# Optimization experiments

Measured on AMD Instinct MI355X. Metric: run time of the kernel, lower is better.

## Reference

```python
import jax, jax.numpy as jnp
import numpy as np

NUM_AGENTS = 8
OBSERVATION_SIZE = 30
INPUT_SHAPE = 4 + 2 * OBSERVATION_SIZE  # 64
STATE_SHAPE = INPUT_SHAPE * NUM_AGENTS  # 512
HYPER_HIDDEN_DIM = 40
QMIX_HIDDEN_DIM = 40


def setup_inputs() -> dict:
    key = jax.random.key(0)
    ks = jax.random.split(key, 16)
    E, T = 256, 256

    def lin(k, fan_in, fan_out):
        kw, kb = jax.random.split(k)
        bound = 1.0 / np.sqrt(fan_in)
        w = jax.random.uniform(kw, (fan_in, fan_out), jnp.float32, -bound, bound)
        b = jax.random.uniform(kb, (fan_out,), jnp.float32, -bound, bound)
        return w, b

    hw1_w0, hw1_b0 = lin(ks[0], STATE_SHAPE, HYPER_HIDDEN_DIM)
    hw1_w1, hw1_b1 = lin(ks[1], HYPER_HIDDEN_DIM, NUM_AGENTS * QMIX_HIDDEN_DIM)
    hw2_w0, hw2_b0 = lin(ks[2], STATE_SHAPE, HYPER_HIDDEN_DIM)
    hw2_w1, hw2_b1 = lin(ks[3], HYPER_HIDDEN_DIM, QMIX_HIDDEN_DIM)
    hb1_w, hb1_b = lin(ks[4], STATE_SHAPE, QMIX_HIDDEN_DIM)
    hb2_w0, hb2_b0 = lin(ks[5], STATE_SHAPE, QMIX_HIDDEN_DIM)
    hb2_w1, hb2_b1 = lin(ks[6], QMIX_HIDDEN_DIM, 1)

    return {
        "q_values": jax.random.normal(ks[7], (E, T, NUM_AGENTS), jnp.float32),
        "states": jax.random.normal(ks[8], (E, T, STATE_SHAPE), jnp.float32),
        "hw1_w0": hw1_w0, "hw1_b0": hw1_b0, "hw1_w1": hw1_w1, "hw1_b1": hw1_b1,
        "hw2_w0": hw2_w0, "hw2_b0": hw2_b0, "hw2_w1": hw2_w1, "hw2_b1": hw2_b1,
        "hb1_w": hb1_w, "hb1_b": hb1_b,
        "hb2_w0": hb2_w0, "hb2_b0": hb2_b0, "hb2_w1": hb2_w1, "hb2_b1": hb2_b1,
    }


def reference(q_values, states, hw1_w0, hw1_b0, hw1_w1, hw1_b1,
              hw2_w0, hw2_b0, hw2_w1, hw2_b1,
              hb1_w, hb1_b, hb2_w0, hb2_b0, hb2_w1, hb2_b1):
    E = q_values.shape[0]
    q = q_values.reshape(-1, NUM_AGENTS)          # [B, A]
    s = states.reshape(-1, STATE_SHAPE)           # [B, S]

    # hyper_w1: Linear-ReLU-Linear -> abs -> [B, A, H]
    w1 = jnp.abs(jax.nn.relu(s @ hw1_w0 + hw1_b0) @ hw1_w1 + hw1_b1)
    w1 = w1.reshape(-1, NUM_AGENTS, QMIX_HIDDEN_DIM)
    b1 = s @ hb1_w + hb1_b                        # [B, H]

    hidden = jax.nn.elu(jnp.einsum('ba,bah->bh', q, w1) + b1)  # [B, H]

    # hyper_w2 -> abs -> [B, H]; hyper_b2 -> [B, 1]
    w2 = jnp.abs(jax.nn.relu(s @ hw2_w0 + hw2_b0) @ hw2_w1 + hw2_b1)
    b2 = jax.nn.relu(s @ hb2_w0 + hb2_b0) @ hb2_w1 + hb2_b1    # [B, 1]

    q_total = jnp.einsum('bh,bh->b', hidden, w2)[:, None] + b2  # [B, 1]
    return q_total.reshape(E, -1, 1)
```

## Files before the change

kernel.cpp:

```cpp
#include <hip/hip_runtime.h>
#include <math.h>

#define NA 8
#define SS 512
#define BROWS 32
#define NTHREADS 320

typedef __attribute__((ext_vector_type(8))) short bf16x8;
typedef __attribute__((ext_vector_type(4))) float f32x4;

static __device__ __forceinline__ unsigned short f2bf(float f) {
    union { float f; unsigned u; } v; v.f = f;
    unsigned r = v.u + 0x7FFFu + ((v.u >> 16) & 1u);
    return (unsigned short)(r >> 16);
}
static __device__ __forceinline__ float bf2f(unsigned short u) {
    union { unsigned u; float f; } v; v.u = ((unsigned)u) << 16; return v.f;
}

#define BP_OFF   0
#define BP1_OFF  81920
#define BP2_OFF  102400
#define BIAS0_BYTE 210944

__global__ void prep_kernel(const float* __restrict__ hw1_w0, const float* __restrict__ hb1_w,
                            const float* __restrict__ hw2_w0, const float* __restrict__ hb2_w0,
                            const float* __restrict__ hw1_w1, const float* __restrict__ hw2_w1,
                            const float* __restrict__ hw1_b0, const float* __restrict__ hb1_b,
                            const float* __restrict__ hw2_b0, const float* __restrict__ hb2_b0,
                            unsigned short* __restrict__ ws16, float* __restrict__ bias0) {
    int idx = blockIdx.x * blockDim.x + threadIdx.x;
    if (idx < 81920) {
        int i = idx & 7, l = (idx >> 3) & 63, t = idx >> 9;
        int kt = t & 15, nt = t >> 4;
        int k = kt * 32 + (l >> 4) * 8 + i;
        int n = nt * 16 + (l & 15);
        int seg = n / 40, c = n - seg * 40;
        const float* src = (seg == 0) ? hw1_w0 : (seg == 1) ? hb1_w : (seg == 2) ? hw2_w0 : hb2_w0;
        ws16[BP_OFF + idx] = f2bf(src[k * 40 + c]);
    } else if (idx < 81920 + 20480) {
        int j = idx - 81920;
        int i = j & 7, l = (j >> 3) & 63, t = j >> 9;
        int kt = t & 1, nt = t >> 1;
        int k = kt * 32 + (l >> 4) * 8 + i;
        int n = nt * 16 + (l & 15);
        float v = (k < 40) ? hw1_w1[k * 320 + n] : 0.f;
        ws16[BP1_OFF + j] = f2bf(v);
    } else if (idx < 81920 + 20480 + 3072) {
        int j = idx - 102400;
        int i = j & 7, l = (j >> 3) & 63, t = j >> 9;
        int kt = t & 1, nt = t >> 1;
        int k = kt * 32 + (l >> 4) * 8 + i;
        int n = nt * 16 + (l & 15);
        float v = (k < 40 && n < 40) ? hw2_w1[k * 40 + n] : 0.f;
        ws16[BP2_OFF + j] = f2bf(v);
    } else if (idx < 81920 + 20480 + 3072 + 160) {
        int j = idx - 105472;
        int seg = j / 40, c = j - seg * 40;
        const float* b = (seg == 0) ? hw1_b0 : (seg == 1) ? hb1_b : (seg == 2) ? hw2_b0 : hb2_b0;
        bias0[j] = b[c];
    }
}

#define W1_STRIDE 324
#define B1_OFF    32768
#define H1_OFF    38400
#define H2_OFF    42496
#define W2_OFF    46592
#define B2_OFF    49152
#define SMEM_BYTES 49408

__global__ __launch_bounds__(NTHREADS, 4) void qmix_kernel(
    const float* __restrict__ q_values, const float* __restrict__ states,
    const unsigned short* __restrict__ Bp, const unsigned short* __restrict__ Bp1,
    const unsigned short* __restrict__ Bp2, const float* __restrict__ bias0,
    const float* __restrict__ hw1_b1, const float* __restrict__ hw2_b1,
    const float* __restrict__ hb2_w1, const float* __restrict__ hb2_b1,
    float* __restrict__ out)
{
    __shared__ __align__(16) char smem[SMEM_BYTES];
    const int tid = threadIdx.x;
    const int wv = tid >> 6;
    const int l = tid & 63;
    const int p = l & 15;
    const int row0 = blockIdx.x * BROWS;

    {
        const float4* sg = (const float4*)(states + (size_t)row0 * SS);
        for (int idx = tid; idx < BROWS * (SS / 4); idx += NTHREADS) {
            int r = idx >> 7;
            int c4 = idx & 127;
            float4 v = sg[idx];
            ushort4 b;
            b.x = f2bf(v.x); b.y = f2bf(v.y); b.z = f2bf(v.z); b.w = f2bf(v.w);
            int byte = (r * 1024 + c4 * 8) ^ ((r & 7) << 4);
            *(ushort4*)(smem + byte) = b;
        }
        for (int idx = tid; idx < 32 * 24; idx += NTHREADS) {
            int r = idx / 24, k = 40 + (idx - r * 24);
            int byte = (r * 128 + k * 2) ^ ((r & 7) << 4);
            *(unsigned short*)(smem + H1_OFF + byte) = 0;
            *(unsigned short*)(smem + H2_OFF + byte) = 0;
        }
    }
    __syncthreads();

    f32x4 acc[2][2] = {};
    {
        const int kch = (l >> 4) * 16;
        const int r0 = p;
        const int r1 = r0 + 16;
        const int swz0 = (r0 & 7) << 4;
        const unsigned short* bp0 = Bp + (size_t)((wv * 2 + 0) * 16) * 512 + (size_t)l * 8;
        const unsigned short* bp1 = Bp + (size_t)((wv * 2 + 1) * 16) * 512 + (size_t)l * 8;
        #pragma unroll
        for (int kt = 0; kt < 16; ++kt) {
            bf16x8 a0 = *(const bf16x8*)(smem + ((r0 * 1024 + kt * 64 + kch) ^ swz0));
            bf16x8 a1 = *(const bf16x8*)(smem + ((r1 * 1024 + kt * 64 + kch) ^ swz0));
            bf16x8 b0 = *(const bf16x8*)(bp0 + kt * 512);
            bf16x8 b1 = *(const bf16x8*)(bp1 + kt * 512);
            acc[0][0] = __builtin_amdgcn_mfma_f32_16x16x32_bf16(a0, b0, acc[0][0], 0, 0, 0);
            acc[0][1] = __builtin_amdgcn_mfma_f32_16x16x32_bf16(a0, b1, acc[0][1], 0, 0, 0);
            acc[1][0] = __builtin_amdgcn_mfma_f32_16x16x32_bf16(a1, b0, acc[1][0], 0, 0, 0);
            acc[1][1] = __builtin_amdgcn_mfma_f32_16x16x32_bf16(a1, b1, acc[1][1], 0, 0, 0);
        }
    }

    {
        float rs[2][4] = {{0.f,0.f,0.f,0.f},{0.f,0.f,0.f,0.f}};
        float* b1buf = (float*)(smem + B1_OFF);
        #pragma unroll
        for (int ntl = 0; ntl < 2; ++ntl) {
            const int c = wv * 32 + ntl * 16 + p;
            const float bia = bias0[c];
            const float hbw = (c >= 120) ? hb2_w1[c - 120] : 0.f;
            #pragma unroll
            for (int mt = 0; mt < 2; ++mt)
            #pragma unroll
            for (int g = 0; g < 4; ++g) {
                const int row = mt * 16 + (l >> 4) * 4 + g;
                const float v = acc[mt][ntl][g] + bia;
                if (c < 40) {
                    *(unsigned short*)(smem + H1_OFF + ((row * 128 + c * 2) ^ ((row & 7) << 4)))
                        = f2bf(fmaxf(v, 0.f));
                } else if (c < 80) {
                    b1buf[row * 44 + (c - 40)] = v;
                } else if (c < 120) {
                    *(unsigned short*)(smem + H2_OFF + ((row * 128 + (c - 80) * 2) ^ ((row & 7) << 4)))
                        = f2bf(fmaxf(v, 0.f));
                } else {
                    rs[mt][g] += fmaxf(v, 0.f) * hbw;
                }
            }
        }
        if (wv >= 3) {
            float* B2 = (float*)(smem + B2_OFF);
            #pragma unroll
            for (int mt = 0; mt < 2; ++mt)
            #pragma unroll
            for (int g = 0; g < 4; ++g) {
                float r2 = rs[mt][g];
                r2 += __shfl_xor(r2, 1);
                r2 += __shfl_xor(r2, 2);
                r2 += __shfl_xor(r2, 4);
                r2 += __shfl_xor(r2, 8);
                if (p == 0) B2[(wv - 3) * 32 + mt * 16 + (l >> 4) * 4 + g] = r2;
            }
        }
    }
    __syncthreads();

    {
        char* H1 = smem + H1_OFF;
        const int kch = (l >> 4) * 16;
        f32x4 wacc[2][4] = {};
        #pragma unroll
        for (int kt = 0; kt < 2; ++kt) {
            bf16x8 a[2];
            #pragma unroll
            for (int mt = 0; mt < 2; ++mt) {
                int row = mt * 16 + p;
                a[mt] = *(const bf16x8*)(H1 + ((row * 128 + kt * 64 + kch) ^ ((row & 7) << 4)));
            }
            #pragma unroll
            for (int t = 0; t < 4; ++t) {
                int nt1 = wv * 4 + t;
                bf16x8 b = *(const bf16x8*)(Bp1 + ((size_t)(nt1 * 2 + kt) * 64 + l) * 8);
                wacc[0][t] = __builtin_amdgcn_mfma_f32_16x16x32_bf16(a[0], b, wacc[0][t], 0, 0, 0);
                wacc[1][t] = __builtin_amdgcn_mfma_f32_16x16x32_bf16(a[1], b, wacc[1][t], 0, 0, 0);
            }
        }
        unsigned short* W1 = (unsigned short*)smem;
        #pragma unroll
        for (int mt = 0; mt < 2; ++mt)
        #pragma unroll
        for (int t = 0; t < 4; ++t)
        #pragma unroll
        for (int g = 0; g < 4; ++g) {
            int row = mt * 16 + (l >> 4) * 4 + g;
            int n = (wv * 4 + t) * 16 + p;
            W1[row * W1_STRIDE + n] = f2bf(fabsf(wacc[mt][t][g] + hw1_b1[n]));
        }
        if (wv < 3) {
            char* H2 = smem + H2_OFF;
            f32x4 c2[2] = {};
            #pragma unroll
            for (int kt = 0; kt < 2; ++kt) {
                bf16x8 a[2];
                #pragma unroll
                for (int mt = 0; mt < 2; ++mt) {
                    int row = mt * 16 + p;
                    a[mt] = *(const bf16x8*)(H2 + ((row * 128 + kt * 64 + kch) ^ ((row & 7) << 4)));
                }
                bf16x8 b = *(const bf16x8*)(Bp2 + ((size_t)(wv * 2 + kt) * 64 + l) * 8);
                c2[0] = __builtin_amdgcn_mfma_f32_16x16x32_bf16(a[0], b, c2[0], 0, 0, 0);
                c2[1] = __builtin_amdgcn_mfma_f32_16x16x32_bf16(a[1], b, c2[1], 0, 0, 0);
            }
            unsigned short* W2 = (unsigned short*)(smem + W2_OFF);
            #pragma unroll
            for (int mt = 0; mt < 2; ++mt)
            #pragma unroll
            for (int g = 0; g < 4; ++g) {
                int row = mt * 16 + (l >> 4) * 4 + g;
                int n = wv * 16 + p;
                if (n < 40) W2[row * 40 + n] = f2bf(fabsf(c2[mt][g] + hw2_b1[n]));
            }
        }
    }
    __syncthreads();

    {
        float* b1buf = (float*)(smem + B1_OFF);
        unsigned short* W1 = (unsigned short*)smem;
        unsigned short* W2 = (unsigned short*)(smem + W2_OFF);
        float* PR = (float*)(smem + H1_OFF);
        int r = tid / 10;
        int hb_ = tid - r * 10;
        const float4* qp = (const float4*)(q_values + (size_t)(row0 + r) * NA);
        float4 qa = qp[0], qb = qp[1];
        float qv[8] = {qa.x, qa.y, qa.z, qa.w, qb.x, qb.y, qb.z, qb.w};
        float psum = 0.f;
        #pragma unroll
        for (int kk = 0; kk < 4; ++kk) {
            int h = hb_ + kk * 10;
            float acc2 = b1buf[r * 44 + h];
            #pragma unroll
            for (int a = 0; a < 8; ++a) acc2 += qv[a] * bf2f(W1[r * W1_STRIDE + a * 40 + h]);
            float hid = (acc2 > 0.f) ? acc2 : expm1f(acc2);
            psum += hid * bf2f(W2[r * 40 + h]);
        }
        PR[tid] = psum;
    }
    __syncthreads();
    if (tid < 32) {
        float* PR = (float*)(smem + H1_OFF);
        float* B2 = (float*)(smem + B2_OFF);
        float s = B2[tid] + B2[32 + tid] + hb2_b1[0];
        #pragma unroll
        for (int g = 0; g < 10; ++g) s += PR[tid * 10 + g];
        out[row0 + tid] = s;
    }
}

extern "C" void kernel_launch(void* const* d_in, const int* in_sizes, int n_in,
                              void* d_out, int out_size, void* d_ws, size_t ws_size,
                              hipStream_t stream) {
    const float* q_values = (const float*)d_in[0];
    const float* states   = (const float*)d_in[1];
    const float* hw1_w0 = (const float*)d_in[2];
    const float* hw1_b0 = (const float*)d_in[3];
    const float* hw1_w1 = (const float*)d_in[4];
    const float* hw1_b1 = (const float*)d_in[5];
    const float* hw2_w0 = (const float*)d_in[6];
    const float* hw2_b0 = (const float*)d_in[7];
    const float* hw2_w1 = (const float*)d_in[8];
    const float* hw2_b1 = (const float*)d_in[9];
    const float* hb1_w  = (const float*)d_in[10];
    const float* hb1_b  = (const float*)d_in[11];
    const float* hb2_w0 = (const float*)d_in[12];
    const float* hb2_b0 = (const float*)d_in[13];
    const float* hb2_w1 = (const float*)d_in[14];
    const float* hb2_b1 = (const float*)d_in[15];

    unsigned short* ws16 = (unsigned short*)d_ws;
    float* bias0 = (float*)((char*)d_ws + BIAS0_BYTE);

    const int prep_total = 81920 + 20480 + 3072 + 160;
    prep_kernel<<<(prep_total + 255) / 256, 256, 0, stream>>>(
        hw1_w0, hb1_w, hw2_w0, hb2_w0, hw1_w1, hw2_w1,
        hw1_b0, hb1_b, hw2_b0, hb2_b0, ws16, bias0);

    const int B = in_sizes[0] / NA;
    qmix_kernel<<<B / BROWS, NTHREADS, 0, stream>>>(
        q_values, states,
        ws16 + BP_OFF, ws16 + BP1_OFF, ws16 + BP2_OFF, bias0,
        hw1_b1, hw2_b1, hb2_w1, hb2_b1, (float*)d_out);
}
```

Baseline: 268.7 us.

## Rewrite qmix kernel as single-wave 16-row blocks with register-resident A operand

Replaces the 320-thread, 32-row block with a single 64-lane wave handling 16 rows. States are loaded straight from global into bf16 MFMA A-fragments held in registers rather than staged through LDS. Biases are folded into the accumulator initialisation, the W1 result is consumed in registers through a bucketed q-weighted reduction, and all __syncthreads are removed. Each wave now streams the full hyper-weight matrix on its own, so weight reads per row double and register pressure rises in exchange for less LDS traffic and no block barriers.

```diff
diff --git a/kernel.cpp b/kernel.cpp
--- a/kernel.cpp
+++ b/kernel.cpp
@@ -3,8 +3,6 @@
 
 #define NA 8
 #define SS 512
-#define BROWS 32
-#define NTHREADS 320
 
 typedef __attribute__((ext_vector_type(8))) short bf16x8;
 typedef __attribute__((ext_vector_type(4))) float f32x4;
@@ -16,6 +14,10 @@
 }
 static __device__ __forceinline__ float bf2f(unsigned short u) {
     union { unsigned u; float f; } v; v.u = ((unsigned)u) << 16; return v.f;
+}
+static __device__ __forceinline__ unsigned pkhu(float x, float y) {
+    union { float f; unsigned u; } a, b; a.f = x; b.f = y;
+    return ((a.u + 0x8000u) >> 16) | ((b.u + 0x8000u) & 0xFFFF0000u);
 }
 
 #define BP_OFF   0
@@ -62,15 +64,14 @@
     }
 }
 
-#define W1_STRIDE 324
-#define B1_OFF    32768
-#define H1_OFF    38400
-#define H2_OFF    42496
-#define W2_OFF    46592
-#define B2_OFF    49152
-#define SMEM_BYTES 49408
-
-__global__ __launch_bounds__(NTHREADS, 4) void qmix_kernel(
+#define LDS_H1 0
+#define LDS_H2 2048
+#define LDS_B1 4096
+#define LDS_W2 6720
+#define LDS_QB 8000
+#define SMEM_BYTES 8512
+
+__global__ __launch_bounds__(64, 4) void qmix_kernel(
     const float* __restrict__ q_values, const float* __restrict__ states,
     const unsigned short* __restrict__ Bp, const unsigned short* __restrict__ Bp1,
     const unsigned short* __restrict__ Bp2, const float* __restrict__ bias0,
@@ -79,186 +80,206 @@
     float* __restrict__ out)
 {
     __shared__ __align__(16) char smem[SMEM_BYTES];
-    const int tid = threadIdx.x;
-    const int wv = tid >> 6;
-    const int l = tid & 63;
-    const int p = l & 15;
-    const int row0 = blockIdx.x * BROWS;
-
+    const int l = threadIdx.x;
+    const int s = l & 15;
+    const int g4 = l >> 4;
+    const int row0 = blockIdx.x * 16;
+
+    if (l < 32) {
+        float4 v = *(const float4*)(q_values + (size_t)row0 * NA + l * 4);
+        *(float4*)(smem + LDS_QB + l * 16) = v;
+    }
+    #pragma unroll
+    for (int i = 0; i < 6; ++i) {
+        int idx = i * 64 + l;
+        int r = idx / 24, k = 40 + idx % 24;
+        int byte = (r * 128 + k * 2) ^ ((r & 7) << 4);
+        *(unsigned short*)(smem + LDS_H1 + byte) = 0;
+        *(unsigned short*)(smem + LDS_H2 + byte) = 0;
+    }
+
+    const float* Ap = states + (size_t)(row0 + s) * SS + g4 * 8;
+    bf16x8 aB[16];
     {
-        const float4* sg = (const float4*)(states + (size_t)row0 * SS);
-        for (int idx = tid; idx < BROWS * (SS / 4); idx += NTHREADS) {
-            int r = idx >> 7;
-            int c4 = idx & 127;
-            float4 v = sg[idx];
-            ushort4 b;
-            b.x = f2bf(v.x); b.y = f2bf(v.y); b.z = f2bf(v.z); b.w = f2bf(v.w);
-            int byte = (r * 1024 + c4 * 8) ^ ((r & 7) << 4);
-            *(ushort4*)(smem + byte) = b;
-        }
-        for (int idx = tid; idx < 32 * 24; idx += NTHREADS) {
-            int r = idx / 24, k = 40 + (idx - r * 24);
-            int byte = (r * 128 + k * 2) ^ ((r & 7) << 4);
-            *(unsigned short*)(smem + H1_OFF + byte) = 0;
-            *(unsigned short*)(smem + H2_OFF + byte) = 0;
-        }
-    }
-    __syncthreads();
-
-    f32x4 acc[2][2] = {};
+        float4 wx[4], wy[4];
+        #pragma unroll
+        for (int d = 0; d < 4; ++d) {
+            wx[d] = *(const float4*)(Ap + d * 32);
+            wy[d] = *(const float4*)(Ap + d * 32 + 4);
+        }
+        #pragma unroll
+        for (int kt = 0; kt < 16; ++kt) {
+            float4 x = wx[kt & 3], y = wy[kt & 3];
+            if (kt + 4 < 16) {
+                wx[kt & 3] = *(const float4*)(Ap + (kt + 4) * 32);
+                wy[kt & 3] = *(const float4*)(Ap + (kt + 4) * 32 + 4);
+            }
+            union { bf16x8 v; unsigned u[4]; } t;
+            t.u[0] = pkhu(x.x, x.y); t.u[1] = pkhu(x.z, x.w);
+            t.u[2] = pkhu(y.x, y.y); t.u[3] = pkhu(y.z, y.w);
+            aB[kt] = t.v;
+        }
+    }
+
+    float rs[4] = {0.f, 0.f, 0.f, 0.f};
+
+    #pragma unroll
+    for (int half = 0; half < 2; ++half) {
+        f32x4 acc[5];
+        #pragma unroll
+        for (int n = 0; n < 5; ++n) {
+            float bv = bias0[(5 * half + n) * 16 + s];
+            acc[n] = (f32x4){bv, bv, bv, bv};
+        }
+        const unsigned short* bp = Bp + ((size_t)(5 * half) * 16 * 64 + l) * 8;
+        __builtin_amdgcn_s_setprio(1);
+        #pragma unroll
+        for (int n = 0; n < 5; ++n) {
+            #pragma unroll
+            for (int kt = 0; kt < 16; ++kt) {
+                bf16x8 b = *(const bf16x8*)(bp + (size_t)(n * 16 + kt) * 512);
+                acc[n] = __builtin_amdgcn_mfma_f32_16x16x32_bf16(aB[kt], b, acc[n], 0, 0, 0);
+            }
+        }
+        __builtin_amdgcn_s_setprio(0);
+
+        if (half == 0) {
+            float* B1 = (float*)(smem + LDS_B1);
+            #pragma unroll
+            for (int n = 0; n < 5; ++n) {
+                int c = n * 16 + s;
+                #pragma unroll
+                for (int g = 0; g < 4; ++g) {
+                    int row = g4 * 4 + g;
+                    float v = acc[n][g];
+                    if (c < 40) {
+                        int byte = (row * 128 + c * 2) ^ ((row & 7) << 4);
+                        *(unsigned short*)(smem + LDS_H1 + byte) = f2bf(fmaxf(v, 0.f));
+                    } else {
+                        B1[row * 41 + (c - 40)] = v;
+                    }
+                }
+            }
+        } else {
+            #pragma unroll
+            for (int n = 0; n < 5; ++n) {
+                int c = 80 + n * 16 + s;
+                float hw = (c >= 120) ? hb2_w1[c - 120] : 0.f;
+                #pragma unroll
+                for (int g = 0; g < 4; ++g) {
+                    int row = g4 * 4 + g;
+                    float v = acc[n][g];
+                    if (c < 120) {
+                        int byte = (row * 128 + (c - 80) * 2) ^ ((row & 7) << 4);
+                        *(unsigned short*)(smem + LDS_H2 + byte) = f2bf(fmaxf(v, 0.f));
+                    } else {
+                        rs[g] += fmaxf(v, 0.f) * hw;
+                    }
+                }
+            }
+            #pragma unroll
+            for (int g = 0; g < 4; ++g) {
+                rs[g] += __shfl_xor(rs[g], 1);
+                rs[g] += __shfl_xor(rs[g], 2);
+                rs[g] += __shfl_xor(rs[g], 4);
+                rs[g] += __shfl_xor(rs[g], 8);
+            }
+        }
+    }
+
+    bf16x8 a1[2], a2[2];
+    #pragma unroll
+    for (int kt = 0; kt < 2; ++kt) {
+        int byte = (s * 128 + kt * 64 + g4 * 16) ^ ((s & 7) << 4);
+        a1[kt] = *(const bf16x8*)(smem + LDS_H1 + byte);
+        a2[kt] = *(const bf16x8*)(smem + LDS_H2 + byte);
+    }
+
     {
-        const int kch = (l >> 4) * 16;
-        const int r0 = p;
-        const int r1 = r0 + 16;
-        const int swz0 = (r0 & 7) << 4;
-        const unsigned short* bp0 = Bp + (size_t)((wv * 2 + 0) * 16) * 512 + (size_t)l * 8;
-        const unsigned short* bp1 = Bp + (size_t)((wv * 2 + 1) * 16) * 512 + (size_t)l * 8;
-        #pragma unroll
-        for (int kt = 0; kt < 16; ++kt) {
-            bf16x8 a0 = *(const bf16x8*)(smem + ((r0 * 1024 + kt * 64 + kch) ^ swz0));
-            bf16x8 a1 = *(const bf16x8*)(smem + ((r1 * 1024 + kt * 64 + kch) ^ swz0));
-            bf16x8 b0 = *(const bf16x8*)(bp0 + kt * 512);
-            bf16x8 b1 = *(const bf16x8*)(bp1 + kt * 512);
-            acc[0][0] = __builtin_amdgcn_mfma_f32_16x16x32_bf16(a0, b0, acc[0][0], 0, 0, 0);
-            acc[0][1] = __builtin_amdgcn_mfma_f32_16x16x32_bf16(a0, b1, acc[0][1], 0, 0, 0);
-            acc[1][0] = __builtin_amdgcn_mfma_f32_16x16x32_bf16(a1, b0, acc[1][0], 0, 0, 0);
-            acc[1][1] = __builtin_amdgcn_mfma_f32_16x16x32_bf16(a1, b1, acc[1][1], 0, 0, 0);
-        }
-    }
-
+        unsigned short* W2 = (unsigned short*)(smem + LDS_W2);
+        #pragma unroll
+        for (int nt = 0; nt < 3; ++nt) {
+            int c = nt * 16 + s;
+            float bv = (c < 40) ? hw2_b1[c] : 0.f;
+            f32x4 wa = (f32x4){bv, bv, bv, bv};
+            wa = __builtin_amdgcn_mfma_f32_16x16x32_bf16(
+                a2[0], *(const bf16x8*)(Bp2 + ((size_t)(nt * 2 + 0) * 64 + l) * 8), wa, 0, 0, 0);
+            wa = __builtin_amdgcn_mfma_f32_16x16x32_bf16(
+                a2[1], *(const bf16x8*)(Bp2 + ((size_t)(nt * 2 + 1) * 64 + l) * 8), wa, 0, 0, 0);
+            if (c < 40) {
+                #pragma unroll
+                for (int g = 0; g < 4; ++g)
+                    W2[(g4 * 4 + g) * 40 + c] = f2bf(fabsf(wa[g]));
+            }
+        }
+    }
+
+    float bucket[4][5] = {};
     {
-        float rs[2][4] = {{0.f,0.f,0.f,0.f},{0.f,0.f,0.f,0.f}};
-        float* b1buf = (float*)(smem + B1_OFF);
-        #pragma unroll
-        for (int ntl = 0; ntl < 2; ++ntl) {
-            const int c = wv * 32 + ntl * 16 + p;
-            const float bia = bias0[c];
-            const float hbw = (c >= 120) ? hb2_w1[c - 120] : 0.f;
-            #pragma unroll
-            for (int mt = 0; mt < 2; ++mt)
-            #pragma unroll
-            for (int g = 0; g < 4; ++g) {
-                const int row = mt * 16 + (l >> 4) * 4 + g;
-                const float v = acc[mt][ntl][g] + bia;
-                if (c < 40) {
-                    *(unsigned short*)(smem + H1_OFF + ((row * 128 + c * 2) ^ ((row & 7) << 4)))
-                        = f2bf(fmaxf(v, 0.f));
-                } else if (c < 80) {
-                    b1buf[row * 44 + (c - 40)] = v;
-                } else if (c < 120) {
-                    *(unsigned short*)(smem + H2_OFF + ((row * 128 + (c - 80) * 2) ^ ((row & 7) << 4)))
-                        = f2bf(fmaxf(v, 0.f));
-                } else {
-                    rs[mt][g] += fmaxf(v, 0.f) * hbw;
+        const float* QB = (const float*)(smem + LDS_QB);
+        const bool lo = (s < 8);
+        #pragma unroll
+        for (int ap = 0; ap < 4; ++ap) {
+            #pragma unroll
+            for (int j = 0; j < 5; ++j) {
+                const int nt = ap * 5 + j;
+                const int k0 = (2 * j) % 5;
+                const int k1 = (2 * j + 1) % 5;
+                const int fl0c = (j >= 3) ? 1 : 0;
+                const int fl1c = (j >= 2) ? 1 : 0;
+                int c = nt * 16 + s;
+                float bv = hw1_b1[c];
+                f32x4 wa = (f32x4){bv, bv, bv, bv};
+                wa = __builtin_amdgcn_mfma_f32_16x16x32_bf16(
+                    a1[0], *(const bf16x8*)(Bp1 + ((size_t)(nt * 2 + 0) * 64 + l) * 8), wa, 0, 0, 0);
+                wa = __builtin_amdgcn_mfma_f32_16x16x32_bf16(
+                    a1[1], *(const bf16x8*)(Bp1 + ((size_t)(nt * 2 + 1) * 64 + l) * 8), wa, 0, 0, 0);
+                int a = 2 * ap + (lo ? fl0c : fl1c);
+                #pragma unroll
+                for (int g = 0; g < 4; ++g) {
+                    float w = fabsf(wa[g]);
+                    float qv = QB[(g4 * 4 + g) * 8 + a];
+                    float p = qv * w;
+                    float p0 = lo ? p : 0.f;
+                    bucket[g][k0] += p0;
+                    bucket[g][k1] += (p - p0);
                 }
             }
         }
-        if (wv >= 3) {
-            float* B2 = (float*)(smem + B2_OFF);
-            #pragma unroll
-            for (int mt = 0; mt < 2; ++mt)
-            #pragma unroll
-            for (int g = 0; g < 4; ++g) {
-                float r2 = rs[mt][g];
-                r2 += __shfl_xor(r2, 1);
-                r2 += __shfl_xor(r2, 2);
-                r2 += __shfl_xor(r2, 4);
-                r2 += __shfl_xor(r2, 8);
-                if (p == 0) B2[(wv - 3) * 32 + mt * 16 + (l >> 4) * 4 + g] = r2;
-            }
-        }
-    }
-    __syncthreads();
+    }
+    #pragma unroll
+    for (int g = 0; g < 4; ++g)
+        #pragma unroll
+        for (int k = 0; k < 5; ++k)
+            bucket[g][k] += __shfl_xor(bucket[g][k], 8);
 
     {
-        char* H1 = smem + H1_OFF;
-        const int kch = (l >> 4) * 16;
-        f32x4 wacc[2][4] = {};
-        #pragma unroll
-        for (int kt = 0; kt < 2; ++kt) {
-            bf16x8 a[2];
-            #pragma unroll
-            for (int mt = 0; mt < 2; ++mt) {
-                int row = mt * 16 + p;
-                a[mt] = *(const bf16x8*)(H1 + ((row * 128 + kt * 64 + kch) ^ ((row & 7) << 4)));
-            }
-            #pragma unroll
-            for (int t = 0; t < 4; ++t) {
-                int nt1 = wv * 4 + t;
-                bf16x8 b = *(const bf16x8*)(Bp1 + ((size_t)(nt1 * 2 + kt) * 64 + l) * 8);
-                wacc[0][t] = __builtin_amdgcn_mfma_f32_16x16x32_bf16(a[0], b, wacc[0][t], 0, 0, 0);
-                wacc[1][t] = __builtin_amdgcn_mfma_f32_16x16x32_bf16(a[1], b, wacc[1][t], 0, 0, 0);
-            }
-        }
-        unsigned short* W1 = (unsigned short*)smem;
-        #pragma unroll
-        for (int mt = 0; mt < 2; ++mt)
-        #pragma unroll
-        for (int t = 0; t < 4; ++t)
+        const float* B1 = (const float*)(smem + LDS_B1);
+        const unsigned short* W2 = (const unsigned short*)(smem + LDS_W2);
+        float ps[4] = {0.f, 0.f, 0.f, 0.f};
         #pragma unroll
         for (int g = 0; g < 4; ++g) {
-            int row = mt * 16 + (l >> 4) * 4 + g;
-            int n = (wv * 4 + t) * 16 + p;
-            W1[row * W1_STRIDE + n] = f2bf(fabsf(wacc[mt][t][g] + hw1_b1[n]));
-        }
-        if (wv < 3) {
-            char* H2 = smem + H2_OFF;
-            f32x4 c2[2] = {};
-            #pragma unroll
-            for (int kt = 0; kt < 2; ++kt) {
-                bf16x8 a[2];
-                #pragma unroll
-                for (int mt = 0; mt < 2; ++mt) {
-                    int row = mt * 16 + p;
-                    a[mt] = *(const bf16x8*)(H2 + ((row * 128 + kt * 64 + kch) ^ ((row & 7) << 4)));
-                }
-                bf16x8 b = *(const bf16x8*)(Bp2 + ((size_t)(wv * 2 + kt) * 64 + l) * 8);
-                c2[0] = __builtin_amdgcn_mfma_f32_16x16x32_bf16(a[0], b, c2[0], 0, 0, 0);
-                c2[1] = __builtin_amdgcn_mfma_f32_16x16x32_bf16(a[1], b, c2[1], 0, 0, 0);
-            }
-            unsigned short* W2 = (unsigned short*)(smem + W2_OFF);
-            #pragma unroll
-            for (int mt = 0; mt < 2; ++mt)
-            #pragma unroll
-            for (int g = 0; g < 4; ++g) {
-                int row = mt * 16 + (l >> 4) * 4 + g;
-                int n = wv * 16 + p;
-                if (n < 40) W2[row * 40 + n] = f2bf(fabsf(c2[mt][g] + hw2_b1[n]));
-            }
-        }
-    }
-    __syncthreads();
-
-    {
-        float* b1buf = (float*)(smem + B1_OFF);
-        unsigned short* W1 = (unsigned short*)smem;
-        unsigned short* W2 = (unsigned short*)(smem + W2_OFF);
-        float* PR = (float*)(smem + H1_OFF);
-        int r = tid / 10;
-        int hb_ = tid - r * 10;
-        const float4* qp = (const float4*)(q_values + (size_t)(row0 + r) * NA);
-        float4 qa = qp[0], qb = qp[1];
-        float qv[8] = {qa.x, qa.y, qa.z, qa.w, qb.x, qb.y, qb.z, qb.w};
-        float psum = 0.f;
-        #pragma unroll
-        for (int kk = 0; kk < 4; ++kk) {
-            int h = hb_ + kk * 10;
-            float acc2 = b1buf[r * 44 + h];
-            #pragma unroll
-            for (int a = 0; a < 8; ++a) acc2 += qv[a] * bf2f(W1[r * W1_STRIDE + a * 40 + h]);
-            float hid = (acc2 > 0.f) ? acc2 : expm1f(acc2);
-            psum += hid * bf2f(W2[r * 40 + h]);
-        }
-        PR[tid] = psum;
-    }
-    __syncthreads();
-    if (tid < 32) {
-        float* PR = (float*)(smem + H1_OFF);
-        float* B2 = (float*)(smem + B2_OFF);
-        float s = B2[tid] + B2[32 + tid] + hb2_b1[0];
-        #pragma unroll
-        for (int g = 0; g < 10; ++g) s += PR[tid * 10 + g];
-        out[row0 + tid] = s;
+            int r = g4 * 4 + g;
+            #pragma unroll
+            for (int k = 0; k < 5; ++k) {
+                int h = (l & 7) + 8 * k;
+                float val = bucket[g][k] + B1[r * 41 + h];
+                float hid = (val > 0.f) ? val : expm1f(val);
+                ps[g] += hid * bf2f(W2[r * 40 + h]);
+            }
+        }
+        #pragma unroll
+        for (int g = 0; g < 4; ++g) {
+            ps[g] += __shfl_xor(ps[g], 1);
+            ps[g] += __shfl_xor(ps[g], 2);
+            ps[g] += __shfl_xor(ps[g], 4);
+        }
+        if (s == 0) {
+            float hb2b = hb2_b1[0];
+            #pragma unroll
+            for (int g = 0; g < 4; ++g)
+                out[row0 + g4 * 4 + g] = ps[g] + rs[g] + hb2b;
+        }
     }
 }
 
@@ -291,7 +312,7 @@
         hw1_b0, hb1_b, hw2_b0, hb2_b0, ws16, bias0);
 
     const int B = in_sizes[0] / NA;
-    qmix_kernel<<<B / BROWS, NTHREADS, 0, stream>>>(
+    qmix_kernel<<<B / 16, 64, 0, stream>>>(
         q_values, states,
         ws16 + BP_OFF, ws16 + BP1_OFF, ws16 + BP2_OFF, bias0,
         hw1_b1, hw2_b1, hb2_w1, hb2_b1, (float*)d_out);
```

After: 263.6 us. Within noise of the previous version (-1.9%).
